# Performance work log

Measured on AMD Instinct MI355X. Metric: run time of the kernel, lower is better.

## Reference

```python
import jax, jax.numpy as jnp
import numpy as np

B, C, H, W = 4, 4, 1080, 1920


def setup_inputs() -> dict:
    key = jax.random.key(0)
    k1, k2 = jax.random.split(key)
    frame = jax.random.normal(k1, (B, C, H, W), dtype=jnp.float32)
    flow = jax.random.normal(k2, (B, 2, H, W), dtype=jnp.float32)
    return {"frame": frame, "flow": flow}


def _bilinear_warp(frame, flow):
    # TF-addons style dense_image_warp: sample frame at (y - flow_y, x - flow_x),
    # query points clamped to the image rectangle, bilinear interpolation.
    b, c, h, w = frame.shape
    gy = jnp.arange(h, dtype=flow.dtype)
    gx = jnp.arange(w, dtype=flow.dtype)
    qy = jnp.clip(gy[None, :, None] - flow[:, 0], 0.0, h - 1)  # [B,H,W]
    qx = jnp.clip(gx[None, None, :] - flow[:, 1], 0.0, w - 1)  # [B,H,W]
    y0f = jnp.floor(qy)
    x0f = jnp.floor(qx)
    wy = (qy - y0f)[:, None]  # [B,1,H,W]
    wx = (qx - x0f)[:, None]
    y0 = y0f.astype(jnp.int32)
    x0 = x0f.astype(jnp.int32)
    y1 = jnp.minimum(y0 + 1, h - 1)
    x1 = jnp.minimum(x0 + 1, w - 1)
    ff = frame.reshape(b, c, h * w)

    def gather(y, x):
        idx = (y * w + x).reshape(b, 1, h * w)
        return jnp.take_along_axis(ff, idx, axis=2).reshape(b, c, h, w)

    top = gather(y0, x0) * (1.0 - wx) + gather(y0, x1) * wx
    bot = gather(y1, x0) * (1.0 - wx) + gather(y1, x1) * wx
    return top * (1.0 - wy) + bot * wy


def reference(frame, flow):
    return _bilinear_warp(frame, flow)
```

## Files before the change

### kernel.cpp

```cpp
#include <hip/hip_runtime.h>


#define BB 4
#define CC 4
#define HH 1080
#define WW 1920
#define HW (HH * WW)
#define NPX (BB * HH * WW)
#define WS_BYTES ((size_t)NPX * CC * 2)

#define TW 128
#define TH 12
#define TILES_X (WW / TW)
#define TILES_Y (HH / TH)
#define NBLK_G (BB * TILES_Y * TILES_X)

#define NBLK_P (NPX / 2 / 256)

typedef _Float16 h8 __attribute__((ext_vector_type(8), aligned(8)));
typedef float f32x2 __attribute__((ext_vector_type(2), aligned(4)));

__global__ __launch_bounds__(256) void nhwc_fp16_prepass(
    const float* __restrict__ frame,
    _Float16* __restrict__ ws)
{
    const int n   = blockIdx.x;
    const int blk = (n & 7) * (NBLK_P >> 3) + (n >> 3);
    const int p   = (blk * 256 + threadIdx.x) * 2;
    const int x = p % WW;
    const int t = p / WW;
    const int y = t % HH;
    const int b = t / HH;

    const size_t off = (size_t)(b * CC) * HW + (size_t)y * WW + x;
    h8 o;
#pragma unroll
    for (int c = 0; c < CC; ++c) {
        const f32x2 v = *reinterpret_cast<const f32x2*>(frame + off + (size_t)c * HW);
        o[c]     = (_Float16)v.x;
        o[c + 4] = (_Float16)v.y;
    }
    *reinterpret_cast<h8*>(ws + (size_t)p * 4) = o;
}

__global__ __launch_bounds__(256) void dense_warp_gather(
    const _Float16* __restrict__ ws,
    const float* __restrict__ flow,
    float* __restrict__ out)
{
    const int n   = blockIdx.x;
    const int blk = (n & 7) * (NBLK_G >> 3) + (n >> 3);

    const int txi = blk % TILES_X;
    const int t2  = blk / TILES_X;
    const int tyi = t2 % TILES_Y;
    const int b   = t2 / TILES_Y;

    const int x     = txi * TW + (threadIdx.x & (TW - 1));
    const int rg    = threadIdx.x >> 7;
    const int ybase = tyi * TH + rg * (TH / 2);

    const float* __restrict__ flowy = flow + (size_t)(b * 2) * HW;
    const float* __restrict__ flowx = flowy + HW;
    const _Float16* __restrict__ wsb = ws + (size_t)b * HW * 4;
    float* __restrict__ outb = out + (size_t)(b * CC) * HW;

#pragma unroll
    for (int r = 0; r < TH / 2; ++r) {
        const int y = ybase + r;
        const size_t rowoff = (size_t)y * WW + x;

        const float fy = flowy[rowoff];
        const float fx = flowx[rowoff];

        const float qy  = fminf(fmaxf((float)y - fy, 0.0f), (float)(HH - 1));
        const float qx  = fminf(fmaxf((float)x - fx, 0.0f), (float)(WW - 1));
        const float y0f = floorf(qy);
        const float x0f = floorf(qx);
        const float wy  = qy - y0f;
        float       wx  = qx - x0f;
        const int y0 = (int)y0f;
        const int x0 = (int)x0f;
        const int y1 = min(y0 + 1, HH - 1);

        const bool edge = (x0 > WW - 2);
        const int  xb   = edge ? (WW - 2) : x0;
        if (edge) wx = 1.0f;

        const h8 tp = *reinterpret_cast<const h8*>(wsb + ((size_t)y0 * WW + xb) * 4);
        const h8 bt = *reinterpret_cast<const h8*>(wsb + ((size_t)y1 * WW + xb) * 4);

        const float omwx = 1.0f - wx;
        const float omwy = 1.0f - wy;

#pragma unroll
        for (int c = 0; c < CC; ++c) {
            const float tl = (float)tp[c];
            const float tr = (float)tp[c + 4];
            const float bl = (float)bt[c];
            const float br = (float)bt[c + 4];
            const float top = tl * omwx + tr * wx;
            const float bot = bl * omwx + br * wx;
            const float v   = top * omwy + bot * wy;
            __builtin_nontemporal_store(v, outb + (size_t)c * HW + rowoff);
        }
    }
}

#define NBLK_F (NPX / 256)

__global__ __launch_bounds__(256) void dense_warp_fallback(
    const float* __restrict__ frame,
    const float* __restrict__ flow,
    float* __restrict__ out)
{
    const int n   = blockIdx.x;
    const int blk = (n & 7) * (NBLK_F >> 3) + (n >> 3);
    const int p   = blk * 256 + threadIdx.x;
    const int x = p % WW;
    const int t = p / WW;
    const int y = t % HH;
    const int b = t / HH;

    const size_t rowoff = (size_t)y * WW + x;
    const float fy = flow[(size_t)(b * 2 + 0) * HW + rowoff];
    const float fx = flow[(size_t)(b * 2 + 1) * HW + rowoff];

    const float qy  = fminf(fmaxf((float)y - fy, 0.0f), (float)(HH - 1));
    const float qx  = fminf(fmaxf((float)x - fx, 0.0f), (float)(WW - 1));
    const float y0f = floorf(qy);
    const float x0f = floorf(qx);
    const float wy  = qy - y0f;
    float       wx  = qx - x0f;
    const int y0 = (int)y0f;
    const int x0 = (int)x0f;
    const int y1 = min(y0 + 1, HH - 1);
    const bool edge = (x0 > WW - 2);
    const int  xb   = edge ? (WW - 2) : x0;
    if (edge) wx = 1.0f;

    const int i0 = y0 * WW + xb;
    const int i1 = y1 * WW + xb;
    const float omwx = 1.0f - wx;
    const float omwy = 1.0f - wy;

#pragma unroll
    for (int c = 0; c < CC; ++c) {
        const float* fp = frame + (size_t)(b * CC + c) * HW;
        const f32x2 t2 = *reinterpret_cast<const f32x2*>(fp + i0);
        const f32x2 b2 = *reinterpret_cast<const f32x2*>(fp + i1);
        const float top = t2.x * omwx + t2.y * wx;
        const float bot = b2.x * omwx + b2.y * wx;
        const float v   = top * omwy + bot * wy;
        __builtin_nontemporal_store(v, out + (size_t)(b * CC + c) * HW + rowoff);
    }
}

extern "C" void kernel_launch(void* const* d_in, const int* in_sizes, int n_in,
                              void* d_out, int out_size, void* d_ws, size_t ws_size,
                              hipStream_t stream)
{
    const float* frame = (const float*)d_in[0];
    const float* flow  = (const float*)d_in[1];
    float* out = (float*)d_out;

    if (ws_size >= WS_BYTES && d_ws != nullptr) {
        _Float16* ws = (_Float16*)d_ws;
        nhwc_fp16_prepass<<<NBLK_P, 256, 0, stream>>>(frame, ws);
        dense_warp_gather<<<NBLK_G, 256, 0, stream>>>(ws, flow, out);
    } else {
        dense_warp_fallback<<<NBLK_F, 256, 0, stream>>>(frame, flow, out);
    }
}
```

Baseline: 71.23 us.

## Process four pixels per thread with vectorized flow loads and output stores

Both the fp16 NHWC prepass and the gather kernel now handle four consecutive pixels per thread, using 16-byte loads of frame and flow and 16-byte nontemporal stores of output. The 2D tile mapping of the gather kernel is replaced by a flat row-linear mapping, and block-to-XCD swizzling is generalized to handle block counts not divisible by eight. This aims to cut instruction and memory-transaction overhead, at the risk of losing the 2D cache locality of the previous tiling and of reducing the number of threads available to hide gather latency.

```diff
diff --git a/kernel.cpp b/kernel.cpp
--- a/kernel.cpp
+++ b/kernel.cpp
@@ -8,39 +8,47 @@
 #define HW (HH * WW)
 #define NPX (BB * HH * WW)
 #define WS_BYTES ((size_t)NPX * CC * 2)
-
-#define TW 128
-#define TH 12
-#define TILES_X (WW / TW)
-#define TILES_Y (HH / TH)
-#define NBLK_G (BB * TILES_Y * TILES_X)
-
-#define NBLK_P (NPX / 2 / 256)
+#define NBLK_Q (NPX / 4 / 256)
+#define NBLK_F (NPX / 256)
 
 typedef _Float16 h8 __attribute__((ext_vector_type(8), aligned(8)));
+typedef float f32x4 __attribute__((ext_vector_type(4), aligned(16)));
 typedef float f32x2 __attribute__((ext_vector_type(2), aligned(4)));
+
+__device__ __forceinline__ int xcd_swizzle(int n, int nblk)
+{
+    const int q   = nblk >> 3;
+    const int r   = nblk & 7;
+    const int xcd = n & 7;
+    const int loc = n >> 3;
+    const int base = (xcd < r) ? xcd * (q + 1) : r * (q + 1) + (xcd - r) * q;
+    return base + loc;
+}
 
 __global__ __launch_bounds__(256) void nhwc_fp16_prepass(
     const float* __restrict__ frame,
     _Float16* __restrict__ ws)
 {
-    const int n   = blockIdx.x;
-    const int blk = (n & 7) * (NBLK_P >> 3) + (n >> 3);
-    const int p   = (blk * 256 + threadIdx.x) * 2;
+    const int blk = xcd_swizzle(blockIdx.x, NBLK_Q);
+    const int p   = (blk * 256 + threadIdx.x) * 4;
     const int x = p % WW;
     const int t = p / WW;
     const int y = t % HH;
     const int b = t / HH;
 
     const size_t off = (size_t)(b * CC) * HW + (size_t)y * WW + x;
-    h8 o;
+    h8 o1, o2;
 #pragma unroll
     for (int c = 0; c < CC; ++c) {
-        const f32x2 v = *reinterpret_cast<const f32x2*>(frame + off + (size_t)c * HW);
-        o[c]     = (_Float16)v.x;
-        o[c + 4] = (_Float16)v.y;
+        const f32x4 v = __builtin_nontemporal_load(
+            reinterpret_cast<const f32x4*>(frame + off + (size_t)c * HW));
+        o1[c]     = (_Float16)v.x;
+        o1[c + 4] = (_Float16)v.y;
+        o2[c]     = (_Float16)v.z;
+        o2[c + 4] = (_Float16)v.w;
     }
-    *reinterpret_cast<h8*>(ws + (size_t)p * 4) = o;
+    *reinterpret_cast<h8*>(ws + (size_t)p * 4)     = o1;
+    *reinterpret_cast<h8*>(ws + (size_t)p * 4 + 8) = o2;
 }
 
 __global__ __launch_bounds__(256) void dense_warp_gather(
@@ -48,33 +56,31 @@
     const float* __restrict__ flow,
     float* __restrict__ out)
 {
-    const int n   = blockIdx.x;
-    const int blk = (n & 7) * (NBLK_G >> 3) + (n >> 3);
+    const int blk = xcd_swizzle(blockIdx.x, NBLK_Q);
+    const int p   = (blk * 256 + threadIdx.x) * 4;
+    const int x = p % WW;
+    const int t = p / WW;
+    const int y = t % HH;
+    const int b = t / HH;
 
-    const int txi = blk % TILES_X;
-    const int t2  = blk / TILES_X;
-    const int tyi = t2 % TILES_Y;
-    const int b   = t2 / TILES_Y;
-
-    const int x     = txi * TW + (threadIdx.x & (TW - 1));
-    const int rg    = threadIdx.x >> 7;
-    const int ybase = tyi * TH + rg * (TH / 2);
-
+    const size_t rowoff = (size_t)y * WW + x;
     const float* __restrict__ flowy = flow + (size_t)(b * 2) * HW;
     const float* __restrict__ flowx = flowy + HW;
     const _Float16* __restrict__ wsb = ws + (size_t)b * HW * 4;
     float* __restrict__ outb = out + (size_t)(b * CC) * HW;
 
+    const f32x4 fy4 = *reinterpret_cast<const f32x4*>(flowy + rowoff);
+    const f32x4 fx4 = *reinterpret_cast<const f32x4*>(flowx + rowoff);
+
+    f32x4 res[CC];
+
 #pragma unroll
-    for (int r = 0; r < TH / 2; ++r) {
-        const int y = ybase + r;
-        const size_t rowoff = (size_t)y * WW + x;
-
-        const float fy = flowy[rowoff];
-        const float fx = flowx[rowoff];
+    for (int i = 0; i < 4; ++i) {
+        const float fy = fy4[i];
+        const float fx = fx4[i];
 
         const float qy  = fminf(fmaxf((float)y - fy, 0.0f), (float)(HH - 1));
-        const float qx  = fminf(fmaxf((float)x - fx, 0.0f), (float)(WW - 1));
+        const float qx  = fminf(fmaxf((float)(x + i) - fx, 0.0f), (float)(WW - 1));
         const float y0f = floorf(qy);
         const float x0f = floorf(qx);
         const float wy  = qy - y0f;
@@ -101,21 +107,23 @@
             const float br = (float)bt[c + 4];
             const float top = tl * omwx + tr * wx;
             const float bot = bl * omwx + br * wx;
-            const float v   = top * omwy + bot * wy;
-            __builtin_nontemporal_store(v, outb + (size_t)c * HW + rowoff);
+            res[c][i] = top * omwy + bot * wy;
         }
     }
+
+#pragma unroll
+    for (int c = 0; c < CC; ++c) {
+        __builtin_nontemporal_store(
+            res[c], reinterpret_cast<f32x4*>(outb + (size_t)c * HW + rowoff));
+    }
 }
-
-#define NBLK_F (NPX / 256)
 
 __global__ __launch_bounds__(256) void dense_warp_fallback(
     const float* __restrict__ frame,
     const float* __restrict__ flow,
     float* __restrict__ out)
 {
-    const int n   = blockIdx.x;
-    const int blk = (n & 7) * (NBLK_F >> 3) + (n >> 3);
+    const int blk = xcd_swizzle(blockIdx.x, NBLK_F);
     const int p   = blk * 256 + threadIdx.x;
     const int x = p % WW;
     const int t = p / WW;
@@ -166,8 +174,8 @@
 
     if (ws_size >= WS_BYTES && d_ws != nullptr) {
         _Float16* ws = (_Float16*)d_ws;
-        nhwc_fp16_prepass<<<NBLK_P, 256, 0, stream>>>(frame, ws);
-        dense_warp_gather<<<NBLK_G, 256, 0, stream>>>(ws, flow, out);
+        nhwc_fp16_prepass<<<NBLK_Q, 256, 0, stream>>>(frame, ws);
+        dense_warp_gather<<<NBLK_Q, 256, 0, stream>>>(ws, flow, out);
     } else {
         dense_warp_fallback<<<NBLK_F, 256, 0, stream>>>(frame, flow, out);
     }
```

Result: slower. 81.38 us (+14.2%).
